# Performance work log

Measured on AMD Instinct MI355X. Metric: run time of the kernel, lower is better.

## Reference

```python
import jax, jax.numpy as jnp
import numpy as np

N = 262144   # flattened seq_len * num_agents
D = 256      # d_model
H = 256      # expert_hidden_dim
E = 4        # num_experts
C = 10       # num_classes
K = 2        # top-k


def setup_inputs() -> dict:
    key = jax.random.key(0)
    ks = jax.random.split(key, 8)
    def w(k, shape, fan_in):
        return jax.random.normal(k, shape, dtype=jnp.float32) / np.sqrt(fan_in).astype(np.float32)
    return {
        "x":   jax.random.normal(ks[0], (N, D), dtype=jnp.float32),
        # gate: Linear(D,D) -> GELU -> Linear(D,E)
        "Wg1": w(ks[1], (D, D), D), "bg1": jnp.zeros((D,), jnp.float32),
        "Wg2": w(ks[2], (D, E), D), "bg2": jnp.zeros((E,), jnp.float32),
        # experts (stacked): Linear(D,H) -> GELU -> Linear(H,C)
        "We1": w(ks[3], (E, D, H), D), "be1": jnp.zeros((E, H), jnp.float32),
        "We2": w(ks[4], (E, H, C), H), "be2": jnp.zeros((E, C), jnp.float32),
        # alpha head: Linear(D,H) -> GELU -> Linear(H,C) -> Softplus
        "Wa1": w(ks[5], (D, H), D), "ba1": jnp.zeros((H,), jnp.float32),
        "Wa2": w(ks[6], (H, C), H), "ba2": jnp.zeros((C,), jnp.float32),
    }


def reference(x, Wg1, bg1, Wg2, bg2, We1, be1, We2, be2, Wa1, ba1, Wa2, ba2):
    gelu = lambda v: jax.nn.gelu(v, approximate=False)  # torch nn.GELU default (erf)

    # --- noisy top-k gating (eval mode: no noise, no dropout) ---
    gate_logits = gelu(x @ Wg1 + bg1) @ Wg2 + bg2                      # [N, E]
    top_vals, top_idx = jax.lax.top_k(gate_logits, K)                  # [N, K]
    rows = jnp.arange(x.shape[0])[:, None]
    gw = jnp.zeros_like(gate_logits).at[rows, top_idx].set(top_vals)   # scatter top-k vals, zeros elsewhere
    gate_weights = jax.nn.softmax(gw, axis=-1)                         # softmax over ALL E slots (zeros included)
    load = gate_weights.sum(axis=0)                                    # [E]

    # --- dense expert ensemble ---
    h = gelu(jnp.einsum('nd,edh->neh', x, We1) + be1)                  # [N, E, H]
    expert_out = jnp.einsum('neh,ehc->nec', h, We2) + be2              # [N, E, C]
    logits = jnp.einsum('nec,ne->nc', expert_out, gate_weights)        # [N, C]

    # --- Dirichlet alpha head ---
    alpha = jax.nn.softplus(gelu(x @ Wa1 + ba1) @ Wa2 + ba2) + 1e-6    # [N, C]

    return logits, alpha, gate_weights, load
```

## Files before the change

### kernel.cpp

```cpp
#include <hip/hip_runtime.h>
#include <hip/hip_bf16.h>


typedef _Float16 f16x8 __attribute__((ext_vector_type(8)));
typedef _Float16 f16x4 __attribute__((ext_vector_type(4)));
typedef float    f32x4 __attribute__((ext_vector_type(4)));

static constexpr int    NTOK      = 262144;
static constexpr size_t ALPHA_OFF = (size_t)NTOK * 10;
static constexpr size_t GW_OFF    = (size_t)2 * NTOK * 10;
static constexpr size_t LOAD_OFF  = GW_OFF + (size_t)NTOK * 4;

static constexpr size_t W1F_OFF   = 0;
static constexpr size_t W2F_OFF   = 786432;
static constexpr size_t CNT_OFF   = 835584;
static constexpr size_t LIST_OFF  = 835648;
static constexpr size_t LPART_OFF = 1884224;

static constexpr float DELTA = 0.02f;

__device__ __forceinline__ float gelu_exact(float v){
  return 0.5f * v * (1.0f + erff(v * 0.7071067811865475f));
}
__device__ __forceinline__ float gelu_fast(float v){
  float t = v * v;
  float p = __builtin_fmaf(0.0713548162726f, t, 1.5957691216057f);
  float z = __expf(v * p);
  float r = __builtin_amdgcn_rcpf(z + 1.0f);
  return v - v * r;
}
__device__ __forceinline__ float softplus_fast(float v){
  float z = __expf(v);
  float l = __logf(1.0f + z);
  return (v > 15.0f) ? v : l;
}
__device__ __forceinline__ f32x4 mfma16(f16x8 a, f16x8 b, f32x4 c){
  return __builtin_amdgcn_mfma_f32_16x16x32_f16(a, b, c, 0, 0, 0);
}
__device__ __forceinline__ f16x8 pk8(float4 a, float4 b){
  union { f16x8 v; unsigned u[4]; } r;
  r.u[0] = __builtin_bit_cast(unsigned, __builtin_amdgcn_cvt_pkrtz(a.x, a.y));
  r.u[1] = __builtin_bit_cast(unsigned, __builtin_amdgcn_cvt_pkrtz(a.z, a.w));
  r.u[2] = __builtin_bit_cast(unsigned, __builtin_amdgcn_cvt_pkrtz(b.x, b.y));
  r.u[3] = __builtin_bit_cast(unsigned, __builtin_amdgcn_cvt_pkrtz(b.z, b.w));
  return r.v;
}
__device__ __forceinline__ f16x4 pk4(float a, float b, float c, float d){
  union { f16x4 v; unsigned u[2]; } r;
  r.u[0] = __builtin_bit_cast(unsigned, __builtin_amdgcn_cvt_pkrtz(a, b));
  r.u[1] = __builtin_bit_cast(unsigned, __builtin_amdgcn_cvt_pkrtz(c, d));
  return r.v;
}

__device__ __forceinline__ void topk4(float v0, float v1, float v2, float v3,
                                      float4& gw, float& gap, int& i1, int& i2){
  float m1 = fmaxf(fmaxf(v0, v1), fmaxf(v2, v3));
  i1 = (v0 == m1) ? 0 : (v1 == m1) ? 1 : (v2 == m1) ? 2 : 3;
  float m2 = 0.f; i2 = -1;
  if (0 != i1){ m2 = v0; i2 = 0; }
  if (1 != i1 && (i2 < 0 || v1 > m2)){ m2 = v1; i2 = 1; }
  if (2 != i1 && (i2 < 0 || v2 > m2)){ m2 = v2; i2 = 2; }
  if (3 != i1 && (i2 < 0 || v3 > m2)){ m2 = v3; i2 = 3; }
  float m3 = -3.0e38f;
  if (0 != i1 && 0 != i2) m3 = fmaxf(m3, v0);
  if (1 != i1 && 1 != i2) m3 = fmaxf(m3, v1);
  if (2 != i1 && 2 != i2) m3 = fmaxf(m3, v2);
  if (3 != i1 && 3 != i2) m3 = fmaxf(m3, v3);
  gap = m2 - m3;
  float mm = fmaxf(m1, 0.0f);
  float s0 = (0 == i1 || 0 == i2) ? v0 : 0.0f;
  float s1 = (1 == i1 || 1 == i2) ? v1 : 0.0f;
  float s2 = (2 == i1 || 2 == i2) ? v2 : 0.0f;
  float s3 = (3 == i1 || 3 == i2) ? v3 : 0.0f;
  float e0 = expf(s0 - mm), e1 = expf(s1 - mm), e2 = expf(s2 - mm), e3 = expf(s3 - mm);
  float inv = 1.0f / (e0 + e1 + e2 + e3);
  gw.x = e0 * inv; gw.y = e1 * inv; gw.z = e2 * inv; gw.w = e3 * inv;
}

__global__ void prep_w1f(const float* __restrict__ We1, const float* __restrict__ Wa1,
                         const float* __restrict__ Wg1, _Float16* __restrict__ W1F){
  int idx = blockIdx.x * 256 + threadIdx.x;
  int e = idx >> 13;
  int r = idx & 8191;
  int kc = r >> 10;
  int entry = r & 1023;
  int ht = entry >> 6, ll = entry & 63;
  int h = ht * 16 + (ll & 15);
  int d0 = kc * 32 + ((ll >> 4) << 3);
  f16x8 o;
  #pragma unroll
  for (int j = 0; j < 8; ++j){
    int d = d0 + j;
    float v;
    if (e < 4)       v = We1[e * 65536 + d * 256 + h];
    else if (e == 4) v = Wa1[d * 256 + h];
    else             v = Wg1[d * 256 + h];
    o[j] = (_Float16)v;
  }
  *(f16x8*)&W1F[(size_t)idx * 8] = o;
}

__global__ void prep_w2f(const float* __restrict__ We2, const float* __restrict__ Wa2,
                         const float* __restrict__ Wg2, _Float16* __restrict__ W2F,
                         unsigned int* __restrict__ cntp){
  if (blockIdx.x == 0 && threadIdx.x == 0) *cntp = 0;
  int idx = blockIdx.x * 256 + threadIdx.x;
  int e = idx >> 9;
  int r = idx & 511;
  int k2 = r >> 6, ll = r & 63;
  int c = ll & 15;
  int h0 = k2 * 32 + ((ll >> 4) << 3);
  f16x8 o;
  #pragma unroll
  for (int j = 0; j < 8; ++j){
    int h = h0 + j;
    float v = 0.0f;
    if (e < 4){ if (c < 10) v = We2[e * 2560 + h * 10 + c]; }
    else if (e == 4){ if (c < 10) v = Wa2[h * 10 + c]; }
    else { if (c < 4) v = Wg2[h * 4 + c]; }
    o[j] = (_Float16)v;
  }
  *(f16x8*)&W2F[(size_t)idx * 8] = o;
}

__device__ __forceinline__ void run_l1(const _Float16* __restrict__ w1s,
                                       const unsigned char* __restrict__ xsb,
                                       int w, int l, int l15, int lq,
                                       f32x4 acc[2][4]){
  #pragma unroll
  for (int kc = 0; kc < 8; ++kc){
    f16x8 af[2], bf[4];
    #pragma unroll
    for (int i = 0; i < 2; ++i)
      af[i] = *(const f16x8*)&w1s[(size_t)kc * 8192 + (w + 8 * i) * 512 + l * 8];
    #pragma unroll
    for (int tt = 0; tt < 4; ++tt){
      int lt = tt * 16 + l15;
      bf[tt] = *(const f16x8*)(xsb + lt * 512 +
                 ((kc * 64 + lq * 16) ^ ((lt & 7) << 4)));
    }
    __builtin_amdgcn_s_setprio(1);
    #pragma unroll
    for (int i = 0; i < 2; ++i)
      #pragma unroll
      for (int tt = 0; tt < 4; ++tt)
        acc[i][tt] = mfma16(af[i], bf[tt], acc[i][tt]);
    __builtin_amdgcn_s_setprio(0);
  }
}

__global__ __launch_bounds__(512, 4) void fused_kernel(
    const float* __restrict__ x,
    const _Float16* __restrict__ W1F, const _Float16* __restrict__ W2F,
    const float* __restrict__ bg1, const float* __restrict__ bg2,
    const float* __restrict__ be1, const float* __restrict__ be2,
    const float* __restrict__ ba1, const float* __restrict__ ba2,
    float* __restrict__ out, unsigned int* __restrict__ list,
    unsigned int* __restrict__ cntp, float* __restrict__ lpart){
  __shared__ __align__(16) unsigned char lds[65600];
  unsigned char* xsb = lds;
  unsigned char* hsb = lds + 32768;
  float*        lsum = (float*)(lds + 65536);

  const int tid = threadIdx.x;
  const int w = tid >> 6, l = tid & 63;
  const int l15 = l & 15, lq = l >> 4;
  const size_t t0 = (size_t)blockIdx.x * 64;
  const int tokL = (w & 3) * 16 + l15;
  const int key  = (tokL & 7) << 4;

  {
    int d = (tid & 31) * 8;
    #pragma unroll
    for (int q = 0; q < 4; ++q){
      int tk = q * 16 + (tid >> 5);
      const float* xp = x + (t0 + tk) * 256 + d;
      float4 f0 = *(const float4*)xp;
      float4 f1 = *(const float4*)(xp + 4);
      *(f16x8*)(xsb + tk * 512 + ((d * 2) ^ ((tk & 7) << 4))) = pk8(f0, f1);
    }
  }
  __syncthreads();

  f32x4 lacc = {0,0,0,0};
  float4 gw4 = {0,0,0,0};

  for (int s = 0; s < 6; ++s){
    const int e = (s == 0) ? 5 : (s - 1);
    f32x4 acc[2][4];
    #pragma unroll
    for (int i = 0; i < 2; ++i)
      #pragma unroll
      for (int tt = 0; tt < 4; ++tt){
        acc[i][tt][0]=0.f; acc[i][tt][1]=0.f; acc[i][tt][2]=0.f; acc[i][tt][3]=0.f;
      }
    run_l1(W1F + (size_t)e * 65536, xsb, w, l, l15, lq, acc);
    __syncthreads();

    const float* b1p = (e == 5) ? bg1 : (e < 4 ? be1 + e * 256 : ba1);
    #pragma unroll
    for (int i = 0; i < 2; ++i){
      int hb = (w + 8 * i) * 16 + lq * 4;
      float4 b4 = *(const float4*)&b1p[hb];
      #pragma unroll
      for (int tt = 0; tt < 4; ++tt){
        f16x4 hv = pk4(gelu_fast(acc[i][tt][0] + b4.x),
                       gelu_fast(acc[i][tt][1] + b4.y),
                       gelu_fast(acc[i][tt][2] + b4.z),
                       gelu_fast(acc[i][tt][3] + b4.w));
        int lt = tt * 16 + l15;
        *(f16x4*)(hsb + lt * 512 + ((hb * 2) ^ ((lt & 7) << 4))) = hv;
      }
    }
    __syncthreads();

    f32x4 d2 = {0,0,0,0};
    #pragma unroll
    for (int k2 = 0; k2 < 8; ++k2){
      f16x8 a2 = *(const f16x8*)&W2F[((size_t)(e * 8 + k2) * 64 + l) * 8];
      f16x8 b2 = *(const f16x8*)(hsb + tokL * 512 + ((k2 * 64 + lq * 16) ^ key));
      d2 = mfma16(a2, b2, d2);
    }

    if (s == 0){
      float4 gw = {0,0,0,0};
      float4 lgw = {0,0,0,0};
      int i1 = 0, i2 = 0;
      bool flagged = false;
      if (lq == 0){
        float v0 = d2[0] + bg2[0], v1 = d2[1] + bg2[1];
        float v2 = d2[2] + bg2[2], v3 = d2[3] + bg2[3];
        float gap;
        topk4(v0, v1, v2, v3, gw, gap, i1, i2);
        if (w < 4){
          size_t t = t0 + tokL;
          *(float4*)&out[GW_OFF + t * 4] = gw;
          flagged = (gap < DELTA);
          lgw = gw;
        }
      }
      gw4.x = __shfl(gw.x, l15, 64);
      gw4.y = __shfl(gw.y, l15, 64);
      gw4.z = __shfl(gw.z, l15, 64);
      gw4.w = __shfl(gw.w, l15, 64);
      if (w < 4){
        unsigned long long m = __ballot(flagged);
        int cnt = __popcll(m);
        if (cnt){
          unsigned base = 0;
          if (l == 0) base = atomicAdd(cntp, (unsigned)cnt);
          base = __shfl(base, 0, 64);
          if (flagged){
            unsigned rank = (unsigned)__popcll(m & ((1ull << l) - 1ull));
            list[base + rank] = (unsigned)(t0 + tokL) | (i1 << 18) | (i2 << 20);
          }
        }
        #pragma unroll
        for (int mm = 1; mm < 64; mm <<= 1){
          lgw.x += __shfl_xor(lgw.x, mm, 64); lgw.y += __shfl_xor(lgw.y, mm, 64);
          lgw.z += __shfl_xor(lgw.z, mm, 64); lgw.w += __shfl_xor(lgw.w, mm, 64);
        }
        if (l == 0) *(float4*)&lsum[w * 4] = lgw;
      }
      __syncthreads();
      if (tid < 4)
        lpart[(size_t)blockIdx.x * 4 + tid] =
            lsum[tid] + lsum[4 + tid] + lsum[8 + tid] + lsum[12 + tid];
    } else if (e < 4){
      float gwv = (e == 0) ? gw4.x : (e == 1) ? gw4.y : (e == 2) ? gw4.z : gw4.w;
      #pragma unroll
      for (int r = 0; r < 4; ++r){
        int c = lq * 4 + r;
        float bv = (c < 10) ? be2[e * 10 + c] : 0.0f;
        lacc[r] += gwv * (d2[r] + bv);
      }
    } else {
      if (w < 4){
        size_t t = t0 + tokL;
        #pragma unroll
        for (int r = 0; r < 4; ++r){
          int c = lq * 4 + r;
          if (c < 10)
            out[ALPHA_OFF + t * 10 + c] = softplus_fast(d2[r] + ba2[c]) + 1e-6f;
        }
      }
    }
  }
  if (w < 4){
    size_t t = t0 + tokL;
    #pragma unroll
    for (int r = 0; r < 4; ++r){
      int c = lq * 4 + r;
      if (c < 10) out[t * 10 + c] = lacc[r];
    }
  }
}

__global__ __launch_bounds__(256) void refine_kernel(
    const float* __restrict__ x, const float* __restrict__ Wg1,
    const float* __restrict__ bg1, const float* __restrict__ Wg2,
    const float* __restrict__ bg2,
    const float* __restrict__ We1, const float* __restrict__ be1,
    const float* __restrict__ We2, const float* __restrict__ be2,
    const unsigned int* __restrict__ list, const unsigned int* __restrict__ cntp,
    float* __restrict__ out){
  int cnt = (int)*cntp;
  int l = threadIdx.x & 63;
  int hb = l * 4;
  for (int idx = blockIdx.x * 4 + (threadIdx.x >> 6); idx < cnt;
       idx += gridDim.x * 4){
    unsigned ent = list[idx];
    int t = (int)(ent & 0x3FFFFu);
    int oi1 = (ent >> 18) & 3, oi2 = (ent >> 20) & 3;
    const float* xr = x + (size_t)t * 256;
    float a0 = 0.f, a1 = 0.f, a2 = 0.f, a3 = 0.f;
    #pragma unroll 8
    for (int d = 0; d < 256; ++d){
      float xv = xr[d];
      float4 wv = *(const float4*)&Wg1[d * 256 + hb];
      a0 = fmaf(xv, wv.x, a0); a1 = fmaf(xv, wv.y, a1);
      a2 = fmaf(xv, wv.z, a2); a3 = fmaf(xv, wv.w, a3);
    }
    float4 b4 = *(const float4*)&bg1[hb];
    float g0 = gelu_exact(a0 + b4.x), g1 = gelu_exact(a1 + b4.y);
    float g2 = gelu_exact(a2 + b4.z), g3 = gelu_exact(a3 + b4.w);
    float4 w0 = *(const float4*)&Wg2[(hb + 0) * 4];
    float4 w1 = *(const float4*)&Wg2[(hb + 1) * 4];
    float4 w2 = *(const float4*)&Wg2[(hb + 2) * 4];
    float4 w3 = *(const float4*)&Wg2[(hb + 3) * 4];
    float p0 = g0 * w0.x + g1 * w1.x + g2 * w2.x + g3 * w3.x;
    float p1 = g0 * w0.y + g1 * w1.y + g2 * w2.y + g3 * w3.y;
    float p2 = g0 * w0.z + g1 * w1.z + g2 * w2.z + g3 * w3.z;
    float p3 = g0 * w0.w + g1 * w1.w + g2 * w2.w + g3 * w3.w;
    #pragma unroll
    for (int m = 1; m < 64; m <<= 1){
      p0 += __shfl_xor(p0, m, 64); p1 += __shfl_xor(p1, m, 64);
      p2 += __shfl_xor(p2, m, 64); p3 += __shfl_xor(p3, m, 64);
    }
    float4 gw; float gap; int i1, i2;
    topk4(p0 + bg2[0], p1 + bg2[1], p2 + bg2[2], p3 + bg2[3], gw, gap, i1, i2);
    if (l == 0) *(float4*)&out[GW_OFF + (size_t)t * 4] = gw;
    int oldset = (1 << oi1) | (1 << oi2);
    int newset = (1 << i1) | (1 << i2);
    if (oldset != newset){
      float lg[10];
      #pragma unroll
      for (int c = 0; c < 10; ++c) lg[c] = 0.f;
      for (int e = 0; e < 4; ++e){
        float gwe = (e == 0) ? gw.x : (e == 1) ? gw.y : (e == 2) ? gw.z : gw.w;
        float c0 = 0.f, c1 = 0.f, c2 = 0.f, c3 = 0.f;
        #pragma unroll 8
        for (int d = 0; d < 256; ++d){
          float xv = xr[d];
          float4 wv = *(const float4*)&We1[e * 65536 + d * 256 + hb];
          c0 = fmaf(xv, wv.x, c0); c1 = fmaf(xv, wv.y, c1);
          c2 = fmaf(xv, wv.z, c2); c3 = fmaf(xv, wv.w, c3);
        }
        float4 be = *(const float4*)&be1[e * 256 + hb];
        float h[4];
        h[0] = gelu_exact(c0 + be.x); h[1] = gelu_exact(c1 + be.y);
        h[2] = gelu_exact(c2 + be.z); h[3] = gelu_exact(c3 + be.w);
        #pragma unroll
        for (int r = 0; r < 4; ++r){
          const float* w2p = &We2[e * 2560 + (hb + r) * 10];
          #pragma unroll
          for (int c = 0; c < 10; ++c) lg[c] += gwe * (h[r] * w2p[c]);
        }
      }
      #pragma unroll
      for (int m = 1; m < 64; m <<= 1)
        #pragma unroll
        for (int c = 0; c < 10; ++c) lg[c] += __shfl_xor(lg[c], m, 64);
      if (l == 0){
        #pragma unroll
        for (int c = 0; c < 10; ++c)
          out[(size_t)t * 10 + c] = lg[c] + gw.x * be2[c] + gw.y * be2[10 + c]
                                         + gw.z * be2[20 + c] + gw.w * be2[30 + c];
      }
    }
  }
}

__global__ void reduce_load(const float* __restrict__ lpart, float* __restrict__ out){
  __shared__ float red[64][4];
  int tid = threadIdx.x;
  int e = tid & 3, ch = tid >> 2;
  float s = 0.0f;
  for (int i = 0; i < 64; ++i) s += lpart[(size_t)(ch * 64 + i) * 4 + e];
  red[ch][e] = s;
  __syncthreads();
  if (tid < 4){
    float t = 0.0f;
    for (int c = 0; c < 64; ++c) t += red[c][tid];
    out[LOAD_OFF + tid] = t;
  }
}

extern "C" void kernel_launch(void* const* d_in, const int* in_sizes, int n_in,
                              void* d_out, int out_size, void* d_ws, size_t ws_size,
                              hipStream_t stream){
  const float* x   = (const float*)d_in[0];
  const float* Wg1 = (const float*)d_in[1];
  const float* bg1 = (const float*)d_in[2];
  const float* Wg2 = (const float*)d_in[3];
  const float* bg2 = (const float*)d_in[4];
  const float* We1 = (const float*)d_in[5];
  const float* be1 = (const float*)d_in[6];
  const float* We2 = (const float*)d_in[7];
  const float* be2 = (const float*)d_in[8];
  const float* Wa1 = (const float*)d_in[9];
  const float* ba1 = (const float*)d_in[10];
  const float* Wa2 = (const float*)d_in[11];
  const float* ba2 = (const float*)d_in[12];
  float* out = (float*)d_out;

  _Float16* W1F       = (_Float16*)((char*)d_ws + W1F_OFF);
  _Float16* W2F       = (_Float16*)((char*)d_ws + W2F_OFF);
  unsigned int* cntp  = (unsigned int*)((char*)d_ws + CNT_OFF);
  unsigned int* list  = (unsigned int*)((char*)d_ws + LIST_OFF);
  float* lpart        = (float*)((char*)d_ws + LPART_OFF);

  hipLaunchKernelGGL(prep_w1f, dim3(192), dim3(256), 0, stream, We1, Wa1, Wg1, W1F);
  hipLaunchKernelGGL(prep_w2f, dim3(12),  dim3(256), 0, stream, We2, Wa2, Wg2, W2F, cntp);
  hipLaunchKernelGGL(fused_kernel, dim3(4096), dim3(512), 0, stream,
                     x, W1F, W2F, bg1, bg2, be1, be2, ba1, ba2,
                     out, list, cntp, lpart);
  hipLaunchKernelGGL(refine_kernel, dim3(1024), dim3(256), 0, stream,
                     x, Wg1, bg1, Wg2, bg2, We1, be1, We2, be2, list, cntp, out);
  hipLaunchKernelGGL(reduce_load, dim3(1), dim3(256), 0, stream, lpart, out);
}
```

Before: 579.9 us.

## Halve hidden LDS buffer, split layer-2 into two passes, raise occupancy

The hidden-activation LDS buffer is cut from 32KB to 16KB by writing and consuming the GELU output in two halves, each followed by four layer-2 MFMAs. Launch bounds rise from 4 to 6 blocks per CU, and the swizzle key widens from 8 to 16 rows. Accumulator zeroing is folded into the first MFMA, and the load reduction is rewritten with float4 loads and wave shuffles. Higher occupancy should hide latency better, at the cost of an extra barrier pair per stage and tighter register limits that may cause spills.

```diff
diff --git a/kernel.cpp b/kernel.cpp
--- a/kernel.cpp
+++ b/kernel.cpp
@@ -127,6 +127,7 @@
                                        const unsigned char* __restrict__ xsb,
                                        int w, int l, int l15, int lq,
                                        f32x4 acc[2][4]){
+  const f32x4 z4 = {0.f, 0.f, 0.f, 0.f};
   #pragma unroll
   for (int kc = 0; kc < 8; ++kc){
     f16x8 af[2], bf[4];
@@ -137,19 +138,19 @@
     for (int tt = 0; tt < 4; ++tt){
       int lt = tt * 16 + l15;
       bf[tt] = *(const f16x8*)(xsb + lt * 512 +
-                 ((kc * 64 + lq * 16) ^ ((lt & 7) << 4)));
+                 ((kc * 64 + lq * 16) ^ ((lt & 15) << 4)));
     }
     __builtin_amdgcn_s_setprio(1);
     #pragma unroll
     for (int i = 0; i < 2; ++i)
       #pragma unroll
       for (int tt = 0; tt < 4; ++tt)
-        acc[i][tt] = mfma16(af[i], bf[tt], acc[i][tt]);
+        acc[i][tt] = mfma16(af[i], bf[tt], (kc == 0) ? z4 : acc[i][tt]);
     __builtin_amdgcn_s_setprio(0);
   }
 }
 
-__global__ __launch_bounds__(512, 4) void fused_kernel(
+__global__ __launch_bounds__(512, 6) void fused_kernel(
     const float* __restrict__ x,
     const _Float16* __restrict__ W1F, const _Float16* __restrict__ W2F,
     const float* __restrict__ bg1, const float* __restrict__ bg2,
@@ -157,17 +158,17 @@
     const float* __restrict__ ba1, const float* __restrict__ ba2,
     float* __restrict__ out, unsigned int* __restrict__ list,
     unsigned int* __restrict__ cntp, float* __restrict__ lpart){
-  __shared__ __align__(16) unsigned char lds[65600];
+  __shared__ __align__(16) unsigned char lds[49216];
   unsigned char* xsb = lds;
   unsigned char* hsb = lds + 32768;
-  float*        lsum = (float*)(lds + 65536);
+  float*        lsum = (float*)(lds + 49152);
 
   const int tid = threadIdx.x;
   const int w = tid >> 6, l = tid & 63;
   const int l15 = l & 15, lq = l >> 4;
   const size_t t0 = (size_t)blockIdx.x * 64;
   const int tokL = (w & 3) * 16 + l15;
-  const int key  = (tokL & 7) << 4;
+  const int key  = (tokL & 15) << 4;
 
   {
     int d = (tid & 31) * 8;
@@ -177,7 +178,7 @@
       const float* xp = x + (t0 + tk) * 256 + d;
       float4 f0 = *(const float4*)xp;
       float4 f1 = *(const float4*)(xp + 4);
-      *(f16x8*)(xsb + tk * 512 + ((d * 2) ^ ((tk & 7) << 4))) = pk8(f0, f1);
+      *(f16x8*)(xsb + tk * 512 + ((d * 2) ^ ((tk & 15) << 4))) = pk8(f0, f1);
     }
   }
   __syncthreads();
@@ -188,38 +189,35 @@
   for (int s = 0; s < 6; ++s){
     const int e = (s == 0) ? 5 : (s - 1);
     f32x4 acc[2][4];
-    #pragma unroll
-    for (int i = 0; i < 2; ++i)
+    run_l1(W1F + (size_t)e * 65536, xsb, w, l, l15, lq, acc);
+
+    const float* b1p = (e == 5) ? bg1 : (e < 4 ? be1 + e * 256 : ba1);
+    f32x4 d2 = {0,0,0,0};
+    #pragma unroll
+    for (int p = 0; p < 2; ++p){
+      __syncthreads();
+      {
+        int hb = (w + 8 * p) * 16 + lq * 4;
+        float4 b4 = *(const float4*)&b1p[hb];
+        int lb = (w * 16 + lq * 4) * 2;
+        #pragma unroll
+        for (int tt = 0; tt < 4; ++tt){
+          f16x4 hv = pk4(gelu_fast(acc[p][tt][0] + b4.x),
+                         gelu_fast(acc[p][tt][1] + b4.y),
+                         gelu_fast(acc[p][tt][2] + b4.z),
+                         gelu_fast(acc[p][tt][3] + b4.w));
+          int lt = tt * 16 + l15;
+          *(f16x4*)(hsb + lt * 256 + (lb ^ ((lt & 15) << 4))) = hv;
+        }
+      }
+      __syncthreads();
       #pragma unroll
-      for (int tt = 0; tt < 4; ++tt){
-        acc[i][tt][0]=0.f; acc[i][tt][1]=0.f; acc[i][tt][2]=0.f; acc[i][tt][3]=0.f;
-      }
-    run_l1(W1F + (size_t)e * 65536, xsb, w, l, l15, lq, acc);
-    __syncthreads();
-
-    const float* b1p = (e == 5) ? bg1 : (e < 4 ? be1 + e * 256 : ba1);
-    #pragma unroll
-    for (int i = 0; i < 2; ++i){
-      int hb = (w + 8 * i) * 16 + lq * 4;
-      float4 b4 = *(const float4*)&b1p[hb];
-      #pragma unroll
-      for (int tt = 0; tt < 4; ++tt){
-        f16x4 hv = pk4(gelu_fast(acc[i][tt][0] + b4.x),
-                       gelu_fast(acc[i][tt][1] + b4.y),
-                       gelu_fast(acc[i][tt][2] + b4.z),
-                       gelu_fast(acc[i][tt][3] + b4.w));
-        int lt = tt * 16 + l15;
-        *(f16x4*)(hsb + lt * 512 + ((hb * 2) ^ ((lt & 7) << 4))) = hv;
-      }
-    }
-    __syncthreads();
-
-    f32x4 d2 = {0,0,0,0};
-    #pragma unroll
-    for (int k2 = 0; k2 < 8; ++k2){
-      f16x8 a2 = *(const f16x8*)&W2F[((size_t)(e * 8 + k2) * 64 + l) * 8];
-      f16x8 b2 = *(const f16x8*)(hsb + tokL * 512 + ((k2 * 64 + lq * 16) ^ key));
-      d2 = mfma16(a2, b2, d2);
+      for (int k2h = 0; k2h < 4; ++k2h){
+        int k2 = 4 * p + k2h;
+        f16x8 a2 = *(const f16x8*)&W2F[((size_t)(e * 8 + k2) * 64 + l) * 8];
+        f16x8 b2 = *(const f16x8*)(hsb + tokL * 256 + ((k2h * 64 + lq * 16) ^ key));
+        d2 = mfma16(a2, b2, d2);
+      }
     }
 
     if (s == 0){
@@ -382,18 +380,27 @@
 }
 
 __global__ void reduce_load(const float* __restrict__ lpart, float* __restrict__ out){
-  __shared__ float red[64][4];
+  __shared__ float red[4][4];
   int tid = threadIdx.x;
-  int e = tid & 3, ch = tid >> 2;
-  float s = 0.0f;
-  for (int i = 0; i < 64; ++i) s += lpart[(size_t)(ch * 64 + i) * 4 + e];
-  red[ch][e] = s;
+  const float4* lp = (const float4*)lpart;
+  float4 v = {0,0,0,0};
+  #pragma unroll
+  for (int j = 0; j < 16; ++j){
+    float4 t = lp[tid + 256 * j];
+    v.x += t.x; v.y += t.y; v.z += t.z; v.w += t.w;
+  }
+  #pragma unroll
+  for (int m = 1; m < 64; m <<= 1){
+    v.x += __shfl_xor(v.x, m, 64); v.y += __shfl_xor(v.y, m, 64);
+    v.z += __shfl_xor(v.z, m, 64); v.w += __shfl_xor(v.w, m, 64);
+  }
+  if ((tid & 63) == 0){
+    red[tid >> 6][0] = v.x; red[tid >> 6][1] = v.y;
+    red[tid >> 6][2] = v.z; red[tid >> 6][3] = v.w;
+  }
   __syncthreads();
-  if (tid < 4){
-    float t = 0.0f;
-    for (int c = 0; c < 64; ++c) t += red[c][tid];
-    out[LOAD_OFF + tid] = t;
-  }
+  if (tid < 4)
+    out[LOAD_OFF + tid] = red[0][tid] + red[1][tid] + red[2][tid] + red[3][tid];
 }
 
 extern "C" void kernel_launch(void* const* d_in, const int* in_sizes, int n_in,
```

Result: slower. 702.1 us (+21.1%).
